# Performance work log

Hardware: AMD Instinct MI355X
Metric: run time of the kernel (lower is better)

## Reference

```python
import jax, jax.numpy as jnp
import numpy as np

B, SQ, SD, H = 64, 64, 512, 128


def setup_inputs() -> dict:
    key = jax.random.key(0)
    k1, k2, k3, k4, k5 = jax.random.split(key, 5)
    q = jax.random.normal(k1, (B, SQ, H), dtype=jnp.float32)
    d_pos = jax.random.normal(k2, (B, SD, H), dtype=jnp.float32)
    d_neg = jax.random.normal(k3, (B, SD, H), dtype=jnp.float32)
    mask_pos = jax.random.randint(k4, (B, SD), 0, 2, dtype=jnp.int32).at[:, 0].set(1)
    mask_neg = jax.random.randint(k5, (B, SD), 0, 2, dtype=jnp.int32).at[:, 0].set(1)
    return {"q": q, "d_pos": d_pos, "d_neg": d_neg,
            "mask_pos": mask_pos, "mask_neg": mask_neg}


def _colbert_maxsim(q, d, mask):
    # q: [a, s, h], d: [b, t, h], mask: [b, t] -> scores [a, b]
    simis = jnp.einsum('ash,bth->abst', q, d)            # [a, b, s, t]
    simis = jnp.where(mask[None, :, None, :] == 0, -jnp.inf, simis)
    return simis.max(axis=3).sum(axis=2)                 # max over t, sum over s


def reference(q, d_pos, d_neg, mask_pos, mask_neg):
    # Concatenate pos and in-batch-negative score blocks -> [B, 2B]
    distances = jnp.concatenate(
        [_colbert_maxsim(q, d_pos, mask_pos),
         _colbert_maxsim(q, d_neg, mask_neg)], axis=1)
    labels = jnp.arange(q.shape[0])
    logp = jax.nn.log_softmax(distances, axis=1)
    loss = -jnp.take_along_axis(logp, labels[:, None], axis=1).mean()
    return loss
```

## Files before the change

### kernel.cpp

```cpp
#include <hip/hip_runtime.h>
#include <hip/hip_bf16.h>
#include <math.h>
#include <stdint.h>

#define BB 64
#define SQN 64
#define SDN 512
#define HH 128

typedef __attribute__((ext_vector_type(8))) short bf16x8;
typedef __attribute__((ext_vector_type(16))) float f32x16;

__device__ __forceinline__ short f2bf(float f) {
  union { float f; unsigned u; } x; x.f = f;
  unsigned r = x.u + 0x7fffu + ((x.u >> 16) & 1u);
  return (short)(r >> 16);
}

__device__ __forceinline__ void gl_lds16(const short* g, short* l) {
  __builtin_amdgcn_global_load_lds(
      (const __attribute__((address_space(1))) unsigned int*)g,
      (__attribute__((address_space(3))) unsigned int*)l, 16, 0, 0);
}

__global__ __launch_bounds__(256)
void prep_kernel(const float* __restrict__ q, const float* __restrict__ dp,
                 const float* __restrict__ dn,
                 const int* __restrict__ mp, const int* __restrict__ mn,
                 short* __restrict__ oq, short* __restrict__ od,
                 int* __restrict__ nchunks) {
  const int tid = threadIdx.x;
  if (blockIdx.x < 128) {
    const int bs = blockIdx.x;
    const int side = bs >> 6, b = bs & 63;
    const int* mask = side ? mn : mp;
    const float* srcmat = side ? dn : dp;
    __shared__ int perm_lds[SDN];
    __shared__ int pad_s;
    if (tid < 64) {
      int run = 0;
      #pragma unroll
      for (int it = 0; it < SDN / 64; ++it) {
        int t = it * 64 + tid;
        int m = mask[b * SDN + t];
        unsigned long long bal = __ballot(m != 0);
        int pos = run + __popcll(bal & ((1ull << tid) - 1ull));
        if (m) perm_lds[pos] = t;
        run += (int)__popcll(bal);
      }
      int pad = (run + 127) & ~127;
      for (int j = run + tid; j < pad; j += 64) perm_lds[j] = -1;
      if (tid == 0) { pad_s = pad; nchunks[bs] = pad >> 7; }
    }
    __syncthreads();
    const int pad = pad_s;
    const int l32 = tid & 31;
    #pragma unroll
    for (int it = 0; it < 64; ++it) {
      int j = it * 8 + (tid >> 5);
      if (j < pad) {
        int src_t = perm_lds[j];
        float4 v = make_float4(0.f, 0.f, 0.f, 0.f);
        if (src_t >= 0)
          v = ((const float4*)(srcmat + ((size_t)b * SDN + src_t) * HH))[l32];
        short4 o; o.x = f2bf(v.x); o.y = f2bf(v.y); o.z = f2bf(v.z); o.w = f2bf(v.w);
        *(short4*)&od[((size_t)bs * SDN + j) * HH + l32 * 4] = o;
      }
    }
  } else {
    const int bq = blockIdx.x - 128;
    #pragma unroll
    for (int it = 0; it < 16; ++it) {
      int i = bq * 4096 + it * 256 + tid;
      float4 v = ((const float4*)q)[i];
      short4 o; o.x = f2bf(v.x); o.y = f2bf(v.y); o.z = f2bf(v.z); o.w = f2bf(v.w);
      *(short4*)&oq[i * 4] = o;
    }
  }
}

__global__ __launch_bounds__(256, 2)
void maxsim_kernel(const short* __restrict__ qb,
                   const short* __restrict__ dc,
                   const int* __restrict__ nchunks,
                   float* __restrict__ scores) {
  const int aslc = blockIdx.x;
  const int b    = blockIdx.y;
  const int side = blockIdx.z;
  const short* db = dc + (size_t)(side * BB + b) * SDN * HH;
  const int nch   = nchunks[side * BB + b];

  __shared__ __align__(16) short d_lds[2][128 * 128];

  const int tid = threadIdx.x;
  const int ln  = tid & 63;
  const int w   = tid >> 6;
  const int l31 = ln & 31;
  const int kh  = ln >> 5;
  const int a   = aslc * 4 + w;

  bf16x8 afrag[2][8];
  #pragma unroll
  for (int mt = 0; mt < 2; ++mt) {
    const short* qrow = qb + ((size_t)a * SQN + mt * 32 + l31) * HH + kh * 8;
    #pragma unroll
    for (int kc = 0; kc < 8; ++kc)
      afrag[mt][kc] = *(const bf16x8*)(qrow + kc * 16);
  }

  float rmax[2][16];
  #pragma unroll
  for (int mt = 0; mt < 2; ++mt)
    #pragma unroll
    for (int r = 0; r < 16; ++r) rmax[mt][r] = 0.0f;

  {
    const short* dsrc = db;
    #pragma unroll
    for (int it = 0; it < 8; ++it) {
      int f = it * 256 + tid;
      int row = f >> 4;
      int c = (f & 15) ^ (row & 15);
      gl_lds16(&dsrc[row * HH + c * 8], &d_lds[0][(it * 256 + w * 64) * 8]);
    }
  }
  __syncthreads();

  for (int tc = 0; tc < nch; ++tc) {
    if (tc + 1 < nch) {
      const short* dsrc = db + (size_t)(tc + 1) * 128 * HH;
      short* dst = d_lds[(tc + 1) & 1];
      #pragma unroll
      for (int it = 0; it < 8; ++it) {
        int f = it * 256 + tid;
        int row = f >> 4;
        int c = (f & 15) ^ (row & 15);
        gl_lds16(&dsrc[row * HH + c * 8], &dst[(it * 256 + w * 64) * 8]);
      }
    }

    const short* buf = d_lds[tc & 1];
    #pragma unroll
    for (int tt = 0; tt < 4; ++tt) {
      int trow = tt * 32 + l31;
      int tm = trow & 15;
      const short* bbase = &buf[trow * HH];
      f32x16 acc0 = {0,0,0,0,0,0,0,0,0,0,0,0,0,0,0,0};
      f32x16 acc1 = {0,0,0,0,0,0,0,0,0,0,0,0,0,0,0,0};
      #pragma unroll
      for (int kc = 0; kc < 8; ++kc) {
        int c = (kc * 2 + kh) ^ tm;
        bf16x8 bfrag = *(const bf16x8*)&bbase[c * 8];
        acc0 = __builtin_amdgcn_mfma_f32_32x32x16_bf16(afrag[0][kc], bfrag, acc0, 0, 0, 0);
        acc1 = __builtin_amdgcn_mfma_f32_32x32x16_bf16(afrag[1][kc], bfrag, acc1, 0, 0, 0);
      }
      #pragma unroll
      for (int r = 0; r < 16; ++r) {
        rmax[0][r] = fmaxf(rmax[0][r], acc0[r]);
        rmax[1][r] = fmaxf(rmax[1][r], acc1[r]);
      }
    }
    __syncthreads();
  }

  float s = 0.f;
  #pragma unroll
  for (int mt = 0; mt < 2; ++mt)
    #pragma unroll
    for (int r = 0; r < 16; ++r) {
      float v = rmax[mt][r];
      v = fmaxf(v, __shfl_xor(v, 1));
      v = fmaxf(v, __shfl_xor(v, 2));
      v = fmaxf(v, __shfl_xor(v, 4));
      v = fmaxf(v, __shfl_xor(v, 8));
      v = fmaxf(v, __shfl_xor(v, 16));
      s += v;
    }
  s += __shfl_xor(s, 32);
  if (ln == 0)
    scores[(size_t)a * (2 * BB) + side * BB + b] = s;
}

__global__ __launch_bounds__(1024)
void loss_kernel(const float* __restrict__ scores, float* __restrict__ out) {
  __shared__ float part[16];
  const int tid = threadIdx.x;
  const int ln = tid & 63;
  const int w  = tid >> 6;
  float acc = 0.f;
  #pragma unroll
  for (int i = 0; i < 4; ++i) {
    int r = w * 4 + i;
    float v0 = scores[r * 128 + ln];
    float v1 = scores[r * 128 + 64 + ln];
    float mx = fmaxf(v0, v1);
    #pragma unroll
    for (int off = 32; off >= 1; off >>= 1) mx = fmaxf(mx, __shfl_xor(mx, off));
    float e = __expf(v0 - mx) + __expf(v1 - mx);
    #pragma unroll
    for (int off = 32; off >= 1; off >>= 1) e += __shfl_xor(e, off);
    float lse = mx + __logf(e);
    float diag = __shfl(v0, r);
    acc += lse - diag;
  }
  if (ln == 0) part[w] = acc;
  __syncthreads();
  if (w == 0) {
    float v = (ln < 16) ? part[ln] : 0.f;
    #pragma unroll
    for (int off = 8; off >= 1; off >>= 1) v += __shfl_xor(v, off);
    if (ln == 0) out[0] = v * (1.0f / 64.0f);
  }
}

extern "C" void kernel_launch(void* const* d_in, const int* in_sizes, int n_in,
                              void* d_out, int out_size, void* d_ws, size_t ws_size,
                              hipStream_t stream) {
  const float* q        = (const float*)d_in[0];
  const float* d_pos    = (const float*)d_in[1];
  const float* d_neg    = (const float*)d_in[2];
  const int*   mask_pos = (const int*)d_in[3];
  const int*   mask_neg = (const int*)d_in[4];

  short* q_bf = (short*)d_ws;
  short* d_c  = q_bf + (size_t)BB * SQN * HH;
  int*   nchunks = (int*)(d_c + (size_t)2 * BB * SDN * HH);
  float* scores  = (float*)(nchunks + 128);

  prep_kernel<<<160, 256, 0, stream>>>(q, d_pos, d_neg, mask_pos, mask_neg,
                                       q_bf, d_c, nchunks);

  dim3 grid(16 , BB , 2 );
  maxsim_kernel<<<grid, 256, 0, stream>>>(q_bf, d_c, nchunks, scores);

  loss_kernel<<<1, 1024, 0, stream>>>(scores, (float*)d_out);
}
```

Baseline: 154.6 us.

## Split prep into finer blocks, double q per wave, fuse loss via last-block atomic

```diff
diff --git a/kernel.cpp b/kernel.cpp
--- a/kernel.cpp
+++ b/kernel.cpp
@@ -24,14 +24,16 @@
 }
 
 __global__ __launch_bounds__(256)
-void prep_kernel(const float* __restrict__ q, const float* __restrict__ dp,
-                 const float* __restrict__ dn,
-                 const int* __restrict__ mp, const int* __restrict__ mn,
-                 short* __restrict__ oq, short* __restrict__ od,
-                 int* __restrict__ nchunks) {
+void convert_kernel(const float* __restrict__ q, const float* __restrict__ dp,
+                    const float* __restrict__ dn,
+                    const int* __restrict__ mp, const int* __restrict__ mn,
+                    short* __restrict__ oq, short* __restrict__ od,
+                    int* __restrict__ nchunks, int* __restrict__ counter) {
   const int tid = threadIdx.x;
-  if (blockIdx.x < 128) {
-    const int bs = blockIdx.x;
+  if (blockIdx.x < 2048) {
+    const int gid = blockIdx.x;
+    const int bs  = gid >> 4;
+    const int sub = gid & 15;
     const int side = bs >> 6, b = bs & 63;
     const int* mask = side ? mn : mp;
     const float* srcmat = side ? dn : dp;
@@ -50,14 +52,17 @@
       }
       int pad = (run + 127) & ~127;
       for (int j = run + tid; j < pad; j += 64) perm_lds[j] = -1;
-      if (tid == 0) { pad_s = pad; nchunks[bs] = pad >> 7; }
+      if (tid == 0) {
+        pad_s = pad;
+        if (sub == 0) nchunks[bs] = pad >> 7;
+      }
     }
     __syncthreads();
     const int pad = pad_s;
     const int l32 = tid & 31;
     #pragma unroll
-    for (int it = 0; it < 64; ++it) {
-      int j = it * 8 + (tid >> 5);
+    for (int p = 0; p < 4; ++p) {
+      int j = sub * 32 + p * 8 + (tid >> 5);
       if (j < pad) {
         int src_t = perm_lds[j];
         float4 v = make_float4(0.f, 0.f, 0.f, 0.f);
@@ -68,7 +73,8 @@
       }
     }
   } else {
-    const int bq = blockIdx.x - 128;
+    if (blockIdx.x == 2048 && tid == 0) counter[0] = 0;
+    const int bq = blockIdx.x - 2048;
     #pragma unroll
     for (int it = 0; it < 16; ++it) {
       int i = bq * 4096 + it * 256 + tid;
@@ -83,39 +89,41 @@
 void maxsim_kernel(const short* __restrict__ qb,
                    const short* __restrict__ dc,
                    const int* __restrict__ nchunks,
-                   float* __restrict__ scores) {
+                   float* __restrict__ scores,
+                   int* __restrict__ counter,
+                   float* __restrict__ out) {
   const int aslc = blockIdx.x;
-  const int b    = blockIdx.y;
-  const int side = blockIdx.z;
-  const short* db = dc + (size_t)(side * BB + b) * SDN * HH;
-  const int nch   = nchunks[side * BB + b];
+  const int bs0  = blockIdx.y * 2;
 
   __shared__ __align__(16) short d_lds[2][128 * 128];
+  __shared__ int islast_s;
 
   const int tid = threadIdx.x;
   const int ln  = tid & 63;
   const int w   = tid >> 6;
   const int l31 = ln & 31;
   const int kh  = ln >> 5;
-  const int a   = aslc * 4 + w;
-
-  bf16x8 afrag[2][8];
+  const int a0  = aslc * 8 + w * 2;
+
+  int nchv[2];
+  nchv[0] = nchunks[bs0];
+  nchv[1] = nchunks[bs0 + 1];
+
+  bf16x8 qfrag[2][2][8];
   #pragma unroll
-  for (int mt = 0; mt < 2; ++mt) {
-    const short* qrow = qb + ((size_t)a * SQN + mt * 32 + l31) * HH + kh * 8;
-    #pragma unroll
-    for (int kc = 0; kc < 8; ++kc)
-      afrag[mt][kc] = *(const bf16x8*)(qrow + kc * 16);
-  }
-
-  float rmax[2][16];
-  #pragma unroll
-  for (int mt = 0; mt < 2; ++mt)
-    #pragma unroll
-    for (int r = 0; r < 16; ++r) rmax[mt][r] = 0.0f;
+  for (int al = 0; al < 2; ++al)
+    #pragma unroll
+    for (int half = 0; half < 2; ++half) {
+      const short* qrow = qb + ((size_t)(a0 + al) * SQN + half * 32 + l31) * HH + kh * 8;
+      #pragma unroll
+      for (int kc = 0; kc < 8; ++kc)
+        qfrag[al][half][kc] = *(const bf16x8*)(qrow + kc * 16);
+    }
+
+  float rmax[2][2] = {{0.f, 0.f}, {0.f, 0.f}};
 
   {
-    const short* dsrc = db;
+    const short* dsrc = dc + (size_t)bs0 * SDN * HH;
     #pragma unroll
     for (int it = 0; it < 8; ++it) {
       int f = it * 256 + tid;
@@ -126,10 +134,15 @@
   }
   __syncthreads();
 
-  for (int tc = 0; tc < nch; ++tc) {
-    if (tc + 1 < nch) {
-      const short* dsrc = db + (size_t)(tc + 1) * 128 * HH;
-      short* dst = d_lds[(tc + 1) & 1];
+  int bi = 0, tc = 0, buf = 0;
+  for (;;) {
+    int nbi = bi, ntc = tc + 1;
+    if (ntc == nchv[bi]) { ntc = 0; nbi = bi + 1; }
+    const bool hn = (nbi < 2);
+
+    if (hn) {
+      const short* dsrc = dc + ((size_t)(bs0 + nbi) * SDN + ntc * 128) * HH;
+      short* dst = &d_lds[buf ^ 1][0];
       #pragma unroll
       for (int it = 0; it < 8; ++it) {
         int f = it * 256 + tid;
@@ -139,58 +152,71 @@
       }
     }
 
-    const short* buf = d_lds[tc & 1];
+    const short* bufp = &d_lds[buf][0];
     #pragma unroll
     for (int tt = 0; tt < 4; ++tt) {
       int trow = tt * 32 + l31;
       int tm = trow & 15;
-      const short* bbase = &buf[trow * HH];
-      f32x16 acc0 = {0,0,0,0,0,0,0,0,0,0,0,0,0,0,0,0};
-      f32x16 acc1 = {0,0,0,0,0,0,0,0,0,0,0,0,0,0,0,0};
+      const short* bbase = &bufp[trow * HH];
+      f32x16 acc00 = {0,0,0,0,0,0,0,0,0,0,0,0,0,0,0,0};
+      f32x16 acc01 = {0,0,0,0,0,0,0,0,0,0,0,0,0,0,0,0};
+      f32x16 acc10 = {0,0,0,0,0,0,0,0,0,0,0,0,0,0,0,0};
+      f32x16 acc11 = {0,0,0,0,0,0,0,0,0,0,0,0,0,0,0,0};
       #pragma unroll
       for (int kc = 0; kc < 8; ++kc) {
         int c = (kc * 2 + kh) ^ tm;
-        bf16x8 bfrag = *(const bf16x8*)&bbase[c * 8];
-        acc0 = __builtin_amdgcn_mfma_f32_32x32x16_bf16(afrag[0][kc], bfrag, acc0, 0, 0, 0);
-        acc1 = __builtin_amdgcn_mfma_f32_32x32x16_bf16(afrag[1][kc], bfrag, acc1, 0, 0, 0);
-      }
-      #pragma unroll
-      for (int r = 0; r < 16; ++r) {
-        rmax[0][r] = fmaxf(rmax[0][r], acc0[r]);
-        rmax[1][r] = fmaxf(rmax[1][r], acc1[r]);
-      }
-    }
+        bf16x8 dfrag = *(const bf16x8*)&bbase[c * 8];
+        acc00 = __builtin_amdgcn_mfma_f32_32x32x16_bf16(dfrag, qfrag[0][0][kc], acc00, 0, 0, 0);
+        acc01 = __builtin_amdgcn_mfma_f32_32x32x16_bf16(dfrag, qfrag[0][1][kc], acc01, 0, 0, 0);
+        acc10 = __builtin_amdgcn_mfma_f32_32x32x16_bf16(dfrag, qfrag[1][0][kc], acc10, 0, 0, 0);
+        acc11 = __builtin_amdgcn_mfma_f32_32x32x16_bf16(dfrag, qfrag[1][1][kc], acc11, 0, 0, 0);
+      }
+      float m00 = acc00[0], m01 = acc01[0], m10 = acc10[0], m11 = acc11[0];
+      #pragma unroll
+      for (int r = 1; r < 16; ++r) {
+        m00 = fmaxf(m00, acc00[r]);
+        m01 = fmaxf(m01, acc01[r]);
+        m10 = fmaxf(m10, acc10[r]);
+        m11 = fmaxf(m11, acc11[r]);
+      }
+      rmax[0][0] = fmaxf(rmax[0][0], m00);
+      rmax[0][1] = fmaxf(rmax[0][1], m01);
+      rmax[1][0] = fmaxf(rmax[1][0], m10);
+      rmax[1][1] = fmaxf(rmax[1][1], m11);
+    }
+
+    if (ntc == 0) {
+      #pragma unroll
+      for (int al = 0; al < 2; ++al) {
+        float v0 = fmaxf(rmax[al][0], __shfl_xor(rmax[al][0], 32));
+        float v1 = fmaxf(rmax[al][1], __shfl_xor(rmax[al][1], 32));
+        float s = v0 + v1;
+        s += __shfl_xor(s, 1);  s += __shfl_xor(s, 2);  s += __shfl_xor(s, 4);
+        s += __shfl_xor(s, 8);  s += __shfl_xor(s, 16);
+        if (ln == 0) scores[(size_t)(a0 + al) * (2 * BB) + bs0 + bi] = s;
+        rmax[al][0] = 0.f; rmax[al][1] = 0.f;
+      }
+    }
+
     __syncthreads();
-  }
-
-  float s = 0.f;
-  #pragma unroll
-  for (int mt = 0; mt < 2; ++mt)
-    #pragma unroll
-    for (int r = 0; r < 16; ++r) {
-      float v = rmax[mt][r];
-      v = fmaxf(v, __shfl_xor(v, 1));
-      v = fmaxf(v, __shfl_xor(v, 2));
-      v = fmaxf(v, __shfl_xor(v, 4));
-      v = fmaxf(v, __shfl_xor(v, 8));
-      v = fmaxf(v, __shfl_xor(v, 16));
-      s += v;
-    }
-  s += __shfl_xor(s, 32);
-  if (ln == 0)
-    scores[(size_t)a * (2 * BB) + side * BB + b] = s;
-}
-
-__global__ __launch_bounds__(1024)
-void loss_kernel(const float* __restrict__ scores, float* __restrict__ out) {
-  __shared__ float part[16];
-  const int tid = threadIdx.x;
-  const int ln = tid & 63;
-  const int w  = tid >> 6;
+    if (!hn) break;
+    bi = nbi; tc = ntc; buf ^= 1;
+  }
+
+  __syncthreads();
+  if (tid == 0) {
+    __threadfence();
+    int old = atomicAdd(counter, 1);
+    islast_s = (old == 511);
+  }
+  __syncthreads();
+  if (!islast_s) return;
+  __threadfence();
+
+  __shared__ float part[4];
   float acc = 0.f;
-  #pragma unroll
-  for (int i = 0; i < 4; ++i) {
-    int r = w * 4 + i;
+  for (int i = 0; i < 16; ++i) {
+    int r = w * 16 + i;
     float v0 = scores[r * 128 + ln];
     float v1 = scores[r * 128 + 64 + ln];
     float mx = fmaxf(v0, v1);
@@ -205,12 +231,8 @@
   }
   if (ln == 0) part[w] = acc;
   __syncthreads();
-  if (w == 0) {
-    float v = (ln < 16) ? part[ln] : 0.f;
-    #pragma unroll
-    for (int off = 8; off >= 1; off >>= 1) v += __shfl_xor(v, off);
-    if (ln == 0) out[0] = v * (1.0f / 64.0f);
-  }
+  if (tid == 0)
+    out[0] = (part[0] + part[1] + part[2] + part[3]) * (1.0f / 64.0f);
 }
 
 extern "C" void kernel_launch(void* const* d_in, const int* in_sizes, int n_in,
@@ -226,12 +248,12 @@
   short* d_c  = q_bf + (size_t)BB * SQN * HH;
   int*   nchunks = (int*)(d_c + (size_t)2 * BB * SDN * HH);
   float* scores  = (float*)(nchunks + 128);
-
-  prep_kernel<<<160, 256, 0, stream>>>(q, d_pos, d_neg, mask_pos, mask_neg,
-                                       q_bf, d_c, nchunks);
-
-  dim3 grid(16 , BB , 2 );
-  maxsim_kernel<<<grid, 256, 0, stream>>>(q_bf, d_c, nchunks, scores);
-
-  loss_kernel<<<1, 1024, 0, stream>>>(scores, (float*)d_out);
-}
+  int*   counter = (int*)(scores + BB * 2 * BB);
+
+  convert_kernel<<<2080, 256, 0, stream>>>(q, d_pos, d_neg, mask_pos, mask_neg,
+                                           q_bf, d_c, nchunks, counter);
+
+  dim3 grid(8 , 64 );
+  maxsim_kernel<<<grid, 256, 0, stream>>>(q_bf, d_c, nchunks, scores,
+                                          counter, (float*)d_out);
+}
```

Result: faster. 146.9 us (-5.0%).
